# Kernel tuning notes

Measured on AMD Instinct MI355X. Metric: run time of the kernel, lower is better.

## Reference

```python
import jax, jax.numpy as jnp
import numpy as np

# Fixed production-scale dims (see shape_source)
B, R, WIDTH, T, H, W = 8, 12, 2304, 4, 16, 29
REDUCE, HID, NC, ROI_SP, DEPTH = 1024, 512, 60, 7, 2
SR = 2  # roi_align sampling ratio (fixed; torchvision default -1 is roi-adaptive)


def conv2d(x, w, pad):
    return jax.lax.conv_general_dilated(
        x, w, (1, 1), [(pad, pad), (pad, pad)],
        dimension_numbers=('NCHW', 'OIHW', 'NCHW'))


def maxpool_3x3_s2(x):
    return jax.lax.reduce_window(
        x, -jnp.inf, jax.lax.max, (1, 1, 3, 3), (1, 1, 2, 2),
        [(0, 0), (0, 0), (1, 1), (1, 1)])


def bilinear(img, ys, xs):
    # img [C,h,w]; ys, xs [P] -> [C,P]; matches torchvision bilinear_interpolate
    h, w = img.shape[1], img.shape[2]
    valid = (ys >= -1.0) & (ys <= h) & (xs >= -1.0) & (xs <= w)
    y = jnp.clip(ys, 0.0, h - 1.0)
    x = jnp.clip(xs, 0.0, w - 1.0)
    y0f = jnp.floor(y); x0f = jnp.floor(x)
    iy0 = y0f.astype(jnp.int32); ix0 = x0f.astype(jnp.int32)
    iy1 = jnp.minimum(iy0 + 1, h - 1); ix1 = jnp.minimum(ix0 + 1, w - 1)
    ly = y - y0f; lx = x - x0f; hy = 1.0 - ly; hx = 1.0 - lx
    v00 = img[:, iy0, ix0]; v01 = img[:, iy0, ix1]
    v10 = img[:, iy1, ix0]; v11 = img[:, iy1, ix1]
    out = hy * hx * v00 + hy * lx * v01 + ly * hx * v10 + ly * lx * v11
    return jnp.where(valid[None, :], out, 0.0)


def roi_align_one(img, box):
    # img [C,H,W]; box (x1,y1,x2,y2) in feature coords; aligned=False, scale=1
    x1, y1, x2, y2 = box[0], box[1], box[2], box[3]
    rw = jnp.maximum(x2 - x1, 1.0)
    rh = jnp.maximum(y2 - y1, 1.0)
    bw = rw / ROI_SP; bh = rh / ROI_SP
    g = (jnp.arange(ROI_SP, dtype=jnp.float32)[:, None]
         + (jnp.arange(SR, dtype=jnp.float32)[None, :] + 0.5) / SR).reshape(-1)  # [7*SR]
    ys = y1 + g * bh; xs = x1 + g * bw
    n = ROI_SP * SR
    yy = jnp.repeat(ys, n); xx = jnp.tile(xs, n)
    vals = bilinear(img, yy, xx)                       # [C, n*n]
    vals = vals.reshape(img.shape[0], ROI_SP, SR, ROI_SP, SR)
    return vals.mean(axis=(2, 4))                      # [C,7,7]


def hr2o_layer(x, qw, kw, vw, cw, gamma, beta):
    # x [R, HID, Hp, Wp]; non-local attention across ROIs of one image
    q = conv2d(x, qw, 1)
    k = conv2d(x, kw, 1)
    v = conv2d(x, vw, 1)
    att = jnp.einsum('ichw,jchw->ijhw', q, k) / jnp.sqrt(jnp.float32(HID))
    att = jax.nn.softmax(att, axis=1)                  # softmax over key rois
    virt = jnp.einsum('ijhw,jchw->ichw', att, v)
    mu = virt.mean(axis=(1, 2, 3), keepdims=True)      # GroupNorm(1, HID)
    var = virt.var(axis=(1, 2, 3), keepdims=True)
    virt = (virt - mu) / jnp.sqrt(var + 1e-5)
    virt = virt * gamma[None, :, None, None] + beta[None, :, None, None]
    virt = jax.nn.relu(virt)
    virt = conv2d(virt, cw, 1)                         # mlp_1x1=False -> 3x3 pad 1
    return x + virt                                    # dropout inactive in eval


def setup_inputs() -> dict:
    key = jax.random.key(0)
    ks = jax.random.split(key, 14)
    features = jax.random.normal(ks[0], (B, WIDTH, T, H, W), jnp.float32)
    xy = jax.random.uniform(ks[1], (B, R, 2), minval=0.0, maxval=0.6)
    wh = jax.random.uniform(ks[2], (B, R, 2), minval=0.2, maxval=0.4)
    rois = jnp.concatenate([xy, xy + wh], axis=-1)     # normalized x1,y1,x2,y2

    def w_(k, shape, fan_in):
        return jax.random.normal(k, shape, jnp.float32) * (1.0 / np.sqrt(fan_in))

    return {
        'features': features,
        'rois': rois,
        'conv_reduce_w': w_(ks[3], (REDUCE, WIDTH, 1, 1), WIDTH),
        'conv1_w': w_(ks[4], (HID, 2 * REDUCE, 1, 1), 2 * REDUCE),
        'conv2_w': w_(ks[5], (HID, HID, 3, 3), HID * 9),
        'hr2o_qw': w_(ks[6], (DEPTH, HID, HID, 3, 3), HID * 9),
        'hr2o_kw': w_(ks[7], (DEPTH, HID, HID, 3, 3), HID * 9),
        'hr2o_vw': w_(ks[8], (DEPTH, HID, HID, 3, 3), HID * 9),
        'hr2o_cw': w_(ks[9], (DEPTH, HID, HID, 3, 3), HID * 9),
        'hr2o_gamma': jnp.ones((DEPTH, HID), jnp.float32),
        'hr2o_beta': jnp.zeros((DEPTH, HID), jnp.float32),
        'fc1_w': w_(ks[10], (HID, REDUCE), REDUCE),
        'fc2_w': w_(ks[11], (NC, 2 * HID), 2 * HID),
    }


def reference(features, rois, conv_reduce_w, conv1_w, conv2_w,
              hr2o_qw, hr2o_kw, hr2o_vw, hr2o_cw, hr2o_gamma, hr2o_beta,
              fc1_w, fc2_w):
    feats = features.mean(axis=2)                      # AdaptiveAvgPool3d((1,H,W)) over T
    feats = conv2d(feats, conv_reduce_w, 0)            # [B, REDUCE, H, W]

    scale = jnp.array([W, H, W, H], jnp.float32)
    boxes = rois * scale                               # feature-space coords (detached)
    ra = jax.vmap(lambda img, bxs: jax.vmap(lambda b: roi_align_one(img, b))(bxs))(
        feats, boxes)                                  # [B, R, REDUCE, 7, 7]
    roi_feats = ra.max(axis=(-2, -1)).reshape(B * R, REDUCE)  # MaxPool2d(7)

    # broadcast bg + tiled actor, concat on channels (eff_h=H, eff_w=W)
    bg = jnp.broadcast_to(feats[:, None], (B, R, REDUCE, H, W))
    actor = jnp.broadcast_to(
        roi_feats.reshape(B, R, REDUCE)[..., None, None], (B, R, REDUCE, H, W))
    x = jnp.concatenate([bg, actor], axis=2).reshape(B * R, 2 * REDUCE, H, W)
    x = jax.nn.relu(conv2d(x, conv1_w, 0))             # 1x1
    x = jax.nn.relu(conv2d(x, conv2_w, 0))             # 3x3, Conv2d default pad=0
    x = maxpool_3x3_s2(x)                              # [B*R, HID, 7, 14]
    hp, wp = x.shape[2], x.shape[3]
    x = x.reshape(B, R, HID, hp, wp)
    for d in range(DEPTH):
        x = jax.vmap(lambda xi: hr2o_layer(
            xi, hr2o_qw[d], hr2o_kw[d], hr2o_vw[d], hr2o_cw[d],
            hr2o_gamma[d], hr2o_beta[d]))(x)
    high = x.mean(axis=(-2, -1)).reshape(B * R, HID)   # GAP

    out = jax.nn.relu(roi_feats @ fc1_w.T)
    out = jnp.concatenate([out, high], axis=1)
    return out @ fc2_w.T                               # [B*R, NC]
```

## Files before the change

### kernel.cpp

```cpp
#include <hip/hip_runtime.h>
#include <math.h>

#define BB 8
#define RR 12
#define WIDTH 2304
#define TT 4
#define HH 16
#define WW 29
#define HWIN (HH*WW)
#define REDUCE 1024
#define HID 512
#define NC 60
#define DEPTH 2
#define NIMG (BB*RR)
#define OH2 14
#define OW2 27
#define NSP2 (OH2*OW2)
#define PH 7
#define PW 14
#define NSP (PH*PW)
#define ATT_SCALE 0.044194173824159216f

typedef __attribute__((ext_vector_type(8))) short short8;
typedef __attribute__((ext_vector_type(4))) float floatx4;

__device__ __forceinline__ void split2(float v, unsigned short& h, unsigned short& l)
{
    union { float f; unsigned u; } c; c.f = v;
    unsigned hb = c.u & 0xffff0000u;
    h = (unsigned short)(hb >> 16);
    union { float f; unsigned u; } hc; hc.u = hb;
    float r = v - hc.f;
    union { float f; unsigned u; } rc; rc.f = r;
    unsigned ru = rc.u + 0x7fffu + ((rc.u >> 16) & 1u);
    l = (unsigned short)(ru >> 16);
}

__device__ __forceinline__ void gll16(const void* g, void* l)
{
    __builtin_amdgcn_global_load_lds((const __attribute__((address_space(1))) void*)g,
                                     (__attribute__((address_space(3))) void*)l,
                                     16, 0, 0);
}

#define MFMA3(d, ah_, al_, bh_, bl_) \
    d = __builtin_amdgcn_mfma_f32_16x16x32_bf16(ah_, bh_, d, 0, 0, 0); \
    d = __builtin_amdgcn_mfma_f32_16x16x32_bf16(ah_, bl_, d, 0, 0, 0); \
    d = __builtin_amdgcn_mfma_f32_16x16x32_bf16(al_, bh_, d, 0, 0, 0);

template<int TYPE, int NSEL, bool RELU, bool RESID, int WR>
__global__ __launch_bounds__(256, 2)
void tapr_k(const int4* __restrict__ WA0, const int4* __restrict__ WA1, const int4* __restrict__ WA2,
            const ushort* __restrict__ BH, const ushort* __restrict__ BL,
            const float* __restrict__ Res,
            float* __restrict__ Y0, float* __restrict__ Y1, float* __restrict__ Y2)
{
    __shared__ int4 L[2064 + 16 * WR];
    const int tid = threadIdx.x;

    int ch, zp, nb = 0;
    if (TYPE == 0) { ch = blockIdx.x / 48; zp = blockIdx.x % 48; }
    else { ch = blockIdx.x / 192; int r = blockIdx.x % 192; nb = r / 48; zp = r % 48; }
    int sel = 0, m0;
    if (NSEL == 3) { sel = ch >> 2; m0 = (ch & 3) * 128; }
    else m0 = ch * 128;
    const int z0 = zp * 2;

    const int4* WA = (NSEL == 3) ? (sel == 0 ? WA0 : sel == 1 ? WA1 : WA2) : WA0;
    float* Y = (NSEL == 3) ? (sel == 0 ? Y0 : sel == 1 ? Y1 : Y2) : Y0;

    const int lane = tid & 63, wv = tid >> 6;
    const int lrow = lane >> 4, lcol = lane & 15;
    constexpr long ALO = 294912;
    constexpr long PLSTR = (TYPE == 1) ? 472L * 512 : 160L * 512;
    const int pbase = (TYPE == 1) ? (((nb * 112) >> 5) * 29 + ((nb * 112) & 31)) : 0;

    int pbnf[7];
#pragma unroll
    for (int nf = 0; nf < 7; ++nf) {
        int col = nf * 16 + lcol;
        if (TYPE == 0) pbnf[nf] = col;
        else { int gn = nb * 112 + col; pbnf[nf] = (gn >> 5) * 29 + (gn & 31) - pbase; }
    }

    int uR[3], uPl[3], uZi[3]; bool uV[3];
    const ushort* uSrc[3];
#pragma unroll
    for (int it = 0; it < 3; ++it) {
        int u = tid + it * 256;
        uV[it] = (u < 4 * WR);
        int uu = uV[it] ? u : 0;
        uR[it] = uu % WR; uPl[it] = (uu / WR) & 1; uZi[it] = uu / (2 * WR);
        const ushort* P = uPl[it] ? BL : BH;
        uSrc[it] = P + (size_t)(z0 + uZi[it]) * PLSTR + (size_t)(pbase + uR[it]) * 512;
    }

    floatx4 acc[2][2][7];
#pragma unroll
    for (int zi = 0; zi < 2; ++zi)
#pragma unroll
        for (int mf = 0; mf < 2; ++mf)
#pragma unroll
            for (int nf = 0; nf < 7; ++nf) acc[zi][mf][nf] = (floatx4){0.f, 0.f, 0.f, 0.f};

#define BCOPY(CB) { \
    _Pragma("unroll") \
    for (int it = 0; it < 3; ++it) if (uV[it]) { \
        const int4* s = (const int4*)(uSrc[it] + (size_t)(CB) * 32); \
        int4 t0 = s[0], t1 = s[1], t2 = s[2], t3_ = s[3]; \
        int bse = 2064 + uZi[it] * (8 * WR) + uPl[it] * (4 * WR) + uR[it]; \
        L[bse] = t0; L[bse + WR] = t1; L[bse + 2 * WR] = t2; L[bse + 3 * WR] = t3_; \
    } }

#define ASTAGE(KST, BUF) { \
    int k8 = (KST) * 4; \
    _Pragma("unroll") \
    for (int j = 0; j < 4; ++j) { \
        int h = wv * 4 + j, p = h >> 3, g = (h >> 1) & 3, hf = h & 1; \
        gll16(WA + (p ? ALO : 0) + (long)(k8 + g) * 512 + m0 + hf * 64 + lane, \
              L + (BUF) * 1032 + (p * 4 + g) * 129 + hf * 64); \
    } }

#define COMPUTE(BUF, SHV) { \
    const int4* La = L + (BUF) * 1032; \
    short8 ah[2], al[2]; \
    _Pragma("unroll") \
    for (int mf = 0; mf < 2; ++mf) { \
        int au = lrow * 129 + (wv * 2 + mf) * 16 + lcol; \
        ah[mf] = *(const short8*)(La + au); \
        al[mf] = *(const short8*)(La + 516 + au); \
    } \
    _Pragma("unroll") \
    for (int nf = 0; nf < 7; ++nf) { \
        int spl = pbnf[nf] + (SHV); \
        _Pragma("unroll") \
        for (int zi = 0; zi < 2; ++zi) { \
            const int4* Lb = L + 2064 + zi * (8 * WR) + lrow * WR + spl; \
            short8 bh = *(const short8*)(Lb); \
            short8 bl = *(const short8*)(Lb + 4 * WR); \
            _Pragma("unroll") \
            for (int mf = 0; mf < 2; ++mf) { MFMA3(acc[zi][mf][nf], ah[mf], al[mf], bh, bl) } \
        } \
    } }

    BCOPY(0)
    ASTAGE(0, 0)
    __syncthreads();

    int cur = 0;
    for (int cb = 0; cb < 16; ++cb) {
#pragma unroll
        for (int tap = 0; tap < 9; ++tap) {
            const int kst = cb * 9 + tap;
            const int t3 = tap / 3;
            const int shv = (TYPE == 0) ? (t3 * 16 + (tap - t3 * 3)) : (t3 * 29 + (tap - t3 * 3));
            if (kst < 143) ASTAGE(kst + 1, cur ^ 1)
            COMPUTE(cur, shv)
            __syncthreads();
            cur ^= 1;
        }
        if (cb < 15) {
            BCOPY(cb + 1)
            __syncthreads();
        }
    }

#pragma unroll
    for (int zi = 0; zi < 2; ++zi) {
        const int z = z0 + zi;
#pragma unroll
        for (int mf = 0; mf < 2; ++mf) {
            int m = m0 + wv * 32 + mf * 16 + lrow * 4;
#pragma unroll
            for (int nf = 0; nf < 7; ++nf) {
                int col = nf * 16 + lcol;
                int sp, realn; bool ok;
                if (TYPE == 0) { int oh = col >> 4, ow = col & 15; ok = ow < 14; sp = oh * 14 + ow; realn = 98; }
                else { int gn = nb * 112 + col; int oh = gn >> 5, ow = gn & 31; ok = ow < 27; sp = oh * 27 + ow; realn = 378; }
                if (ok) {
#pragma unroll
                    for (int r = 0; r < 4; ++r) {
                        size_t idx = ((size_t)z * 512 + m + r) * realn + sp;
                        float v = acc[zi][mf][nf][r];
                        if (RESID) v += Res[idx];
                        if (RELU) v = fmaxf(v, 0.f);
                        Y[idx] = v;
                    }
                }
            }
        }
    }
#undef BCOPY
#undef ASTAGE
#undef COMPUTE
}

template<int KW, int KSTN, int MTOT, long PLSTR, int NREAL>
__global__ __launch_bounds__(256, 2)
void tapc_k(const int4* __restrict__ WA,
            const ushort* __restrict__ BH, const ushort* __restrict__ BL,
            float* __restrict__ Y)
{
    __shared__ int4 L[3872];
    const int tid = threadIdx.x;
    const int z = blockIdx.z, nb = blockIdx.x;
    const int m0 = blockIdx.y * 128;
    const int lane = tid & 63, wv = tid >> 6;
    const int lrow = lane >> 4, lcol = lane & 15;
    constexpr long ALO = (long)KSTN * 4 * MTOT;

    int nU[2], gU[2]; long pbU[2]; bool vU[2];
#pragma unroll
    for (int it = 0; it < 2; ++it) {
        int u = tid + (it << 8);
        vU[it] = (u < 448);
        int uu = vU[it] ? u : 0;
        nU[it] = uu % 112; gU[it] = uu / 112;
        int gn = nb * 112 + nU[it];
        pbU[it] = min(gn, NREAL - 1);
    }
    const ushort* BHz = BH + (size_t)z * PLSTR;
    const ushort* BLz = BL + (size_t)z * PLSTR;

    floatx4 acc[2][7];
#pragma unroll
    for (int mf = 0; mf < 2; ++mf)
#pragma unroll
        for (int nf = 0; nf < 7; ++nf) acc[mf][nf] = (floatx4){0.f, 0.f, 0.f, 0.f};

    short8 rbh[2], rbl[2];

#define STAGE_ISSUE(KST, BUF) { \
    int k8 = (KST) * 4; \
    _Pragma("unroll") \
    for (int j = 0; j < 4; ++j) { \
        int h = wv * 4 + j, p = h >> 3, g = (h >> 1) & 3, hf = h & 1; \
        gll16(WA + (p ? ALO : 0) + (long)(k8 + g) * MTOT + m0 + hf * 64 + lane, \
              L + (BUF) * 1936 + (p * 4 + g) * 129 + hf * 64); \
    } \
    int ci0 = (KST) << 5; \
    _Pragma("unroll") \
    for (int it = 0; it < 2; ++it) if (vU[it]) { \
        size_t o = (size_t)pbU[it] * KW + ci0 + gU[it] * 8; \
        rbh[it] = *(const short8*)(BHz + o); \
        rbl[it] = *(const short8*)(BLz + o); \
    } }

#define STAGE_WRITE(BUF) { \
    _Pragma("unroll") \
    for (int it = 0; it < 2; ++it) if (vU[it]) { \
        *((short8*)(L + (BUF) * 1936 + 1032 + gU[it] * 113 + nU[it])) = rbh[it]; \
        *((short8*)(L + (BUF) * 1936 + 1484 + gU[it] * 113 + nU[it])) = rbl[it]; \
    } }

#define COMPUTE(BUF) { \
    const int4* Lc = L + (BUF) * 1936; \
    short8 ah[2], al[2]; \
    _Pragma("unroll") \
    for (int mf = 0; mf < 2; ++mf) { \
        int au = lrow * 129 + (wv * 2 + mf) * 16 + lcol; \
        ah[mf] = *(const short8*)(Lc + au); \
        al[mf] = *(const short8*)(Lc + 516 + au); \
    } \
    _Pragma("unroll") \
    for (int nf = 0; nf < 7; ++nf) { \
        int bu = 1032 + lrow * 113 + nf * 16 + lcol; \
        short8 bh = *(const short8*)(Lc + bu); \
        short8 bl = *(const short8*)(Lc + bu + 452); \
        _Pragma("unroll") \
        for (int mf = 0; mf < 2; ++mf) { MFMA3(acc[mf][nf], ah[mf], al[mf], bh, bl) } \
    } }

    STAGE_ISSUE(0, 0)
    STAGE_WRITE(0)
    __syncthreads();

    int cur = 0;
    for (int kst = 0; kst < KSTN; ++kst) {
        int nxt = cur ^ 1;
        bool more = (kst + 1 < KSTN);
        if (more) STAGE_ISSUE(kst + 1, nxt)
        COMPUTE(cur)
        if (more) { STAGE_WRITE(nxt) __syncthreads(); }
        cur = nxt;
    }

#pragma unroll
    for (int mf = 0; mf < 2; ++mf) {
        int m = m0 + wv * 32 + mf * 16 + lrow * 4;
#pragma unroll
        for (int nf = 0; nf < 7; ++nf) {
            int col = nf * 16 + lcol;
            int gn = nb * 112 + col;
            if (gn < NREAL) {
#pragma unroll
                for (int r = 0; r < 4; ++r) {
                    size_t idx = ((size_t)z * MTOT + m + r) * NREAL + gn;
                    Y[idx] = acc[mf][nf][r];
                }
            }
        }
    }
#undef STAGE_ISSUE
#undef STAGE_WRITE
#undef COMPUTE
}

__global__ void prep_w_k(const float* __restrict__ s0, const float* __restrict__ s1,
                         const float* __restrict__ s2, const float* __restrict__ s3,
                         int4* __restrict__ dst)
{
    const int c = blockIdx.y;
    const float* src = (c == 0) ? s0 : (c == 1) ? s1 : (c == 2) ? s2 : s3;
    int4* dh = dst + (size_t)c * 589824;
    int4* dl = dh + 294912;
    int idx = blockIdx.x * 256 + threadIdx.x;
    if (idx >= 294912) return;
    int g8 = idx / 512, m = idx & 511;
    unsigned hw[4], lw[4];
#pragma unroll
    for (int j = 0; j < 4; ++j) {
        int k1 = g8 * 8 + 2 * j, k2 = k1 + 1;
        int cb1 = k1 / 288, r1 = k1 % 288, tp1 = r1 >> 5, ci1 = cb1 * 32 + (r1 & 31);
        int cb2 = k2 / 288, r2 = k2 % 288, tp2 = r2 >> 5, ci2 = cb2 * 32 + (r2 & 31);
        float v1 = src[(size_t)m * 4608 + ci1 * 9 + tp1];
        float v2 = src[(size_t)m * 4608 + ci2 * 9 + tp2];
        unsigned short h0, l0, h1, l1;
        split2(v1, h0, l0); split2(v2, h1, l1);
        hw[j] = (unsigned)h0 | ((unsigned)h1 << 16);
        lw[j] = (unsigned)l0 | ((unsigned)l1 << 16);
    }
    dh[idx] = make_int4(hw[0], hw[1], hw[2], hw[3]);
    dl[idx] = make_int4(lw[0], lw[1], lw[2], lw[3]);
}

__global__ void prep_wg_k(const float* __restrict__ src, int ldw, int M, int K8,
                          int4* __restrict__ dst)
{
    int idx = blockIdx.x * 256 + threadIdx.x;
    if (idx >= K8 * M) return;
    int g8 = idx / M, m = idx % M;
    unsigned hw[4], lw[4];
#pragma unroll
    for (int j = 0; j < 4; ++j) {
        int k1 = g8 * 8 + 2 * j;
        float v1 = src[(size_t)m * ldw + k1];
        float v2 = src[(size_t)m * ldw + k1 + 1];
        unsigned short h0, l0, h1, l1;
        split2(v1, h0, l0); split2(v2, h1, l1);
        hw[j] = (unsigned)h0 | ((unsigned)h1 << 16);
        lw[j] = (unsigned)l0 | ((unsigned)l1 << 16);
    }
    dst[idx] = make_int4(hw[0], hw[1], hw[2], hw[3]);
    dst[(size_t)K8 * M + idx] = make_int4(lw[0], lw[1], lw[2], lw[3]);
}

__global__ __launch_bounds__(256)
void tsplit_k(const float* __restrict__ src, ushort* __restrict__ dh, ushort* __restrict__ dl,
              int C, int S, long zsrc, long zdst)
{
    __shared__ float t[64][65];
    const int c0 = blockIdx.x * 64, s0 = blockIdx.y * 64, z = blockIdx.z;
    const float* sz = src + (size_t)z * zsrc;
    const int tx = threadIdx.x & 63, ty = threadIdx.x >> 6;
#pragma unroll
    for (int i = 0; i < 16; ++i) {
        int cc = i * 4 + ty;
        int c = c0 + cc, s = s0 + tx;
        t[cc][tx] = (c < C && s < S) ? sz[(size_t)c * S + s] : 0.f;
    }
    __syncthreads();
#pragma unroll
    for (int i = 0; i < 16; ++i) {
        int ss = i * 4 + ty;
        int s = s0 + ss, c = c0 + tx;
        if (s < S && c < C) {
            unsigned short h, l;
            split2(t[tx][ss], h, l);
            size_t o = (size_t)z * zdst + (size_t)s * C + c;
            dh[o] = h; dl[o] = l;
        }
    }
}

__global__ __launch_bounds__(256)
void tsplit_c2_k(const float* __restrict__ bg, const float* __restrict__ bias1,
                 ushort* __restrict__ dh, ushort* __restrict__ dl)
{
    __shared__ float t[64][65];
    const int c0 = blockIdx.x * 64, s0 = blockIdx.y * 64, z = blockIdx.z;
    const int b = z / RR;
    const int tx = threadIdx.x & 63, ty = threadIdx.x >> 6;
#pragma unroll
    for (int i = 0; i < 16; ++i) {
        int cc = i * 4 + ty;
        int s = s0 + tx;
        t[cc][tx] = (s < 464) ? bg[((size_t)b * 512 + c0 + cc) * 464 + s] : 0.f;
    }
    __syncthreads();
    const float bv = bias1[z * 512 + c0 + tx];
#pragma unroll
    for (int i = 0; i < 16; ++i) {
        int ss = i * 4 + ty;
        int s = s0 + ss, c = c0 + tx;
        if (s < 472) {
            float v = (s < 464) ? fmaxf(t[tx][ss] + bv, 0.f) : 0.f;
            unsigned short h, l;
            split2(v, h, l);
            size_t o = (size_t)z * 241664 + (size_t)s * 512 + c;
            dh[o] = h; dl[o] = l;
        }
    }
}

__global__ __launch_bounds__(256)
void tsplit_pad_k(const float* __restrict__ x, ushort* __restrict__ dh, ushort* __restrict__ dl)
{
    __shared__ float t[64 * 99];
    const int c0 = blockIdx.x * 64, z = blockIdx.y;
    const int tid = threadIdx.x;
#pragma unroll
    for (int i = 0; i < 25; ++i) {
        int idx = tid + i * 256;
        if (idx < 6272) {
            int c = idx / 98, s = idx % 98;
            t[c * 99 + s] = x[((size_t)z * 512 + c0 + c) * 98 + s];
        }
    }
    __syncthreads();
#pragma unroll
    for (int i = 0; i < 40; ++i) {
        int idx = tid + i * 256;
        int sp = idx >> 6, c = idx & 63;
        int r = sp >> 4, col = sp & 15;
        float v = (r >= 1 && r <= 7 && col >= 1 && col <= 14) ? t[c * 99 + (r - 1) * 14 + col - 1] : 0.f;
        unsigned short h, l;
        split2(v, h, l);
        size_t o = (size_t)z * 81920 + (size_t)sp * 512 + c0 + c;
        dh[o] = h; dl[o] = l;
    }
}

__global__ void tmean_k(const float* __restrict__ f, float* __restrict__ o, int total)
{
    int i = blockIdx.x * blockDim.x + threadIdx.x;
    if (i >= total) return;
    int p = i % HWIN; long bc = i / HWIN;
    const float* src = f + bc * (long)TT * HWIN + p;
    o[i] = (src[0] + src[HWIN] + src[2 * HWIN] + src[3 * HWIN]) * 0.25f;
}

__global__ __launch_bounds__(256)
void roi_align_k(const float* __restrict__ feats, const float* __restrict__ rois,
                 float* __restrict__ roi_feats)
{
    __shared__ int s_o00[196], s_o01[196], s_o10[196], s_o11[196];
    __shared__ float s_w[4][196];
    const int n = blockIdx.x;
    const int b = n / RR;
    const int t = threadIdx.x;
    if (t < 196) {
        float x1 = rois[n * 4 + 0] * WW, y1 = rois[n * 4 + 1] * HH;
        float x2 = rois[n * 4 + 2] * WW, y2 = rois[n * 4 + 3] * HH;
        float rw = fmaxf(x2 - x1, 1.f), rh = fmaxf(y2 - y1, 1.f);
        float bw = rw / 7.f, bh = rh / 7.f;
        int j = t / 14, i = t % 14;
        float gy = (float)(j >> 1) + ((j & 1) + 0.5f) * 0.5f;
        float gx = (float)(i >> 1) + ((i & 1) + 0.5f) * 0.5f;
        float ys = y1 + gy * bh, xs = x1 + gx * bw;
        bool valid = (ys >= -1.f) && (ys <= (float)HH) && (xs >= -1.f) && (xs <= (float)WW);
        float y = fminf(fmaxf(ys, 0.f), (float)(HH - 1));
        float x = fminf(fmaxf(xs, 0.f), (float)(WW - 1));
        float y0f = floorf(y), x0f = floorf(x);
        int iy0 = (int)y0f, ix0 = (int)x0f;
        int iy1 = min(iy0 + 1, HH - 1), ix1 = min(ix0 + 1, WW - 1);
        float ly = y - y0f, lx = x - x0f, hy = 1.f - ly, hx = 1.f - lx;
        float msk = valid ? 1.f : 0.f;
        s_o00[t] = iy0 * WW + ix0; s_o01[t] = iy0 * WW + ix1;
        s_o10[t] = iy1 * WW + ix0; s_o11[t] = iy1 * WW + ix1;
        s_w[0][t] = hy * hx * msk; s_w[1][t] = hy * lx * msk;
        s_w[2][t] = ly * hx * msk; s_w[3][t] = ly * lx * msk;
    }
    __syncthreads();
    for (int c = t; c < REDUCE; c += 256) {
        const float* img = feats + ((long)(b * REDUCE + c)) * HWIN;
        float mx = -INFINITY;
        for (int bin = 0; bin < 49; ++bin) {
            int by_ = bin / 7, bx = bin % 7;
            float s = 0.f;
#pragma unroll
            for (int sy = 0; sy < 2; ++sy)
#pragma unroll
                for (int sx = 0; sx < 2; ++sx) {
                    int ss = (by_ * 2 + sy) * 14 + bx * 2 + sx;
                    s += s_w[0][ss] * img[s_o00[ss]] + s_w[1][ss] * img[s_o01[ss]]
                       + s_w[2][ss] * img[s_o10[ss]] + s_w[3][ss] * img[s_o11[ss]];
                }
            mx = fmaxf(mx, s * 0.25f);
        }
        roi_feats[(long)n * REDUCE + c] = mx;
    }
}

__global__ void dots_k(const float* __restrict__ Xr, const float* __restrict__ Wt,
                       int ldw, int woff, float* __restrict__ Y,
                       int Nrows, int M, int K, int relu)
{
    int idx = blockIdx.x * blockDim.x + threadIdx.x;
    if (idx >= Nrows * M) return;
    int o = idx / Nrows, n = idx % Nrows;
    const float* xr = Xr + (long)n * K;
    const float* w = Wt + (long)o * ldw + woff;
    float acc = 0.f;
    for (int k = 0; k < K; ++k) acc = fmaf(xr[k], w[k], acc);
    if (relu) acc = fmaxf(acc, 0.f);
    Y[(long)n * M + o] = acc;
}

__global__ void maxpool_k(const float* __restrict__ in, float* __restrict__ out, int total)
{
    int idx = blockIdx.x * blockDim.x + threadIdx.x;
    if (idx >= total) return;
    int ow = idx % PW; int r = idx / PW; int oh = r % PH; long nc = r / PH;
    const float* src = in + nc * NSP2;
    float m = -INFINITY;
    for (int kh = 0; kh < 3; ++kh) {
        int ih = oh * 2 - 1 + kh; if (ih < 0 || ih >= OH2) continue;
        for (int kw = 0; kw < 3; ++kw) {
            int iw = ow * 2 - 1 + kw; if (iw < 0 || iw >= OW2) continue;
            m = fmaxf(m, src[ih * OW2 + iw]);
        }
    }
    out[idx] = m;
}

__global__ __launch_bounds__(256)
void att2_k(const float* __restrict__ q, const float* __restrict__ k, float* __restrict__ att)
{
    __shared__ float qs[5376];
    __shared__ float ks[5376];
    __shared__ float sc[1008];
    const int b = blockIdx.x, p0 = blockIdx.y * 7;
    const int tid = threadIdx.x;

    int itI[4], itJ[4], itP[4]; bool itV[4];
#pragma unroll
    for (int r = 0; r < 4; ++r) {
        int item = tid + (r << 8);
        itV[r] = item < 1008;
        int it = itV[r] ? item : 0;
        int ij = it / 7; itP[r] = it % 7;
        itI[r] = ij / 12; itJ[r] = ij % 12;
    }
    float acc[4] = {0.f, 0.f, 0.f, 0.f};

    for (int cc0 = 0; cc0 < 512; cc0 += 64) {
        for (int l = tid; l < 5376; l += 256) {
            int i = l / 448, r = l % 448, c = r / 7, p = r % 7;
            size_t off = ((size_t)(b * 12 + i) * 512 + cc0 + c) * 98 + p0 + p;
            qs[l] = q[off];
            ks[l] = k[off];
        }
        __syncthreads();
#pragma unroll
        for (int r = 0; r < 4; ++r) {
            if (itV[r]) {
                const float* qp = qs + itI[r] * 448 + itP[r];
                const float* kp = ks + itJ[r] * 448 + itP[r];
                float a = acc[r];
#pragma unroll 8
                for (int c = 0; c < 64; ++c) a = fmaf(qp[c * 7], kp[c * 7], a);
                acc[r] = a;
            }
        }
        __syncthreads();
    }
#pragma unroll
    for (int r = 0; r < 4; ++r)
        if (itV[r]) sc[tid + (r << 8)] = acc[r] * ATT_SCALE;
    __syncthreads();
    if (tid < 84) {
        int i = tid / 7, p = tid % 7;
        float m = -INFINITY;
        float v[12];
#pragma unroll
        for (int j = 0; j < 12; ++j) { v[j] = sc[(i * 12 + j) * 7 + p]; m = fmaxf(m, v[j]); }
        float s = 0.f;
#pragma unroll
        for (int j = 0; j < 12; ++j) { v[j] = expf(v[j] - m); s += v[j]; }
        float inv = 1.f / s;
#pragma unroll
        for (int j = 0; j < 12; ++j)
            att[((size_t)(b * 12 + i) * 12 + j) * 98 + p0 + p] = v[j] * inv;
    }
}

__global__ __launch_bounds__(256)
void virt2_k(const float* __restrict__ att, const float* __restrict__ v, float* __restrict__ virt)
{
    __shared__ float as_[14112];
    const int b = blockIdx.x, cb = blockIdx.y;
    const int tid = threadIdx.x;
    for (int l = tid; l < 14112; l += 256) as_[l] = att[(size_t)b * 14112 + l];
    __syncthreads();

    for (int it = tid; it < 6272; it += 256) {
        int c = cb * 64 + it / 98, p = it % 98;
        float o[12];
#pragma unroll
        for (int i = 0; i < 12; ++i) o[i] = 0.f;
#pragma unroll
        for (int j = 0; j < 12; ++j) {
            float vj = v[((size_t)(b * 12 + j) * 512 + c) * 98 + p];
#pragma unroll
            for (int i = 0; i < 12; ++i) o[i] = fmaf(as_[(i * 12 + j) * 98 + p], vj, o[i]);
        }
#pragma unroll
        for (int i = 0; i < 12; ++i)
            virt[((size_t)(b * 12 + i) * 512 + c) * 98 + p] = o[i];
    }
}

__global__ __launch_bounds__(256)
void stats_k(const float* __restrict__ virt, float* __restrict__ mu, float* __restrict__ rstd)
{
    int n = blockIdx.x;
    const float* src = virt + (long)n * HID * NSP;
    float s = 0.f, q = 0.f;
    for (int i = threadIdx.x; i < HID * NSP; i += 256) {
        float v = src[i]; s += v; q = fmaf(v, v, q);
    }
    for (int off = 32; off; off >>= 1) { s += __shfl_down(s, off); q += __shfl_down(q, off); }
    __shared__ float ss[4], sq[4];
    int w = threadIdx.x >> 6;
    if ((threadIdx.x & 63) == 0) { ss[w] = s; sq[w] = q; }
    __syncthreads();
    if (threadIdx.x == 0) {
        float S = ss[0] + ss[1] + ss[2] + ss[3];
        float Q = sq[0] + sq[1] + sq[2] + sq[3];
        const float invN = 1.f / (HID * NSP);
        float m = S * invN;
        float var = Q * invN - m * m;
        mu[n] = m; rstd[n] = rsqrtf(var + 1e-5f);
    }
}

__global__ void norm_k(float* __restrict__ virt, const float* __restrict__ mu,
                       const float* __restrict__ rstd,
                       const float* __restrict__ gamma, const float* __restrict__ beta)
{
    int idx = blockIdx.x * blockDim.x + threadIdx.x;
    const int TOT = NIMG * HID * NSP;
    if (idx >= TOT) return;
    int n = idx / (HID * NSP);
    int c = (idx / NSP) % HID;
    float val = (virt[idx] - mu[n]) * rstd[n] * gamma[c] + beta[c];
    virt[idx] = fmaxf(val, 0.f);
}

__global__ void meanpool_k(const float* __restrict__ x, float* __restrict__ high)
{
    int idx = blockIdx.x * blockDim.x + threadIdx.x;
    if (idx >= NIMG * HID) return;
    const float* src = x + (long)idx * NSP;
    float s = 0.f;
    for (int p = 0; p < NSP; ++p) s += src[p];
    high[idx] = s * (1.f / NSP);
}

__global__ void final_k(const float* __restrict__ fc1o, const float* __restrict__ high,
                        const float* __restrict__ fc2, float* __restrict__ out)
{
    int idx = blockIdx.x * blockDim.x + threadIdx.x;
    if (idx >= NIMG * NC) return;
    int n = idx / NC, o = idx % NC;
    const float* w = fc2 + (long)o * (2 * HID);
    const float* a = fc1o + (long)n * HID;
    const float* h = high + (long)n * HID;
    float acc = 0.f;
    for (int c = 0; c < HID; ++c) acc = fmaf(a[c], w[c], acc);
    for (int c = 0; c < HID; ++c) acc = fmaf(h[c], w[HID + c], acc);
    out[idx] = acc;
}

extern "C" void kernel_launch(void* const* d_in, const int* in_sizes, int n_in,
                              void* d_out, int out_size, void* d_ws, size_t ws_size,
                              hipStream_t stream)
{
    (void)in_sizes; (void)n_in; (void)out_size; (void)ws_size;
    const float* features = (const float*)d_in[0];
    const float* rois     = (const float*)d_in[1];
    const float* w_reduce = (const float*)d_in[2];
    const float* w_conv1  = (const float*)d_in[3];
    const float* w_conv2  = (const float*)d_in[4];
    const float* qw       = (const float*)d_in[5];
    const float* kw       = (const float*)d_in[6];
    const float* vw       = (const float*)d_in[7];
    const float* cw       = (const float*)d_in[8];
    const float* gamma    = (const float*)d_in[9];
    const float* beta     = (const float*)d_in[10];
    const float* fc1      = (const float*)d_in[11];
    const float* fc2      = (const float*)d_in[12];
    float* ws = (float*)d_ws;

    float*  tmean = ws + 0;
    ushort* tmTH  = (ushort*)(ws + 8552448);
    ushort* tmTL  = (ushort*)(ws + 12828672);
    float*  feats = ws + 17104896;
    ushort* ftTH  = (ushort*)(ws + 0);
    ushort* ftTL  = (ushort*)(ws + 1900544);
    ushort* B2H   = (ushort*)(ws + 0);
    ushort* B2L   = (ushort*)(ws + 11599872);
    int4*   WTQ   = (int4*)(ws + 0);
    float*  bg    = ws + 23199744;
    float*  out2  = ws + 23199744;
    float*  qb    = ws + 23199744;
    float*  kb    = ws + 28016640;
    float*  vb    = ws + 32833536;
    ushort* PTH   = (ushort*)(ws + 41779200);
    ushort* PTL   = (ushort*)(ws + 45711360);
    float*  xb    = ws + 49643520;
    float*  virt  = ws + 54460416;
    int4*   WTS   = (int4*)(ws + 59277312);
    float*  rf    = ws + 61636608;
    float*  bias1 = ws + 61734912;
    float*  fc1o  = ws + 61784064;
    float*  attb  = ws + 61833216;
    float*  mu    = ws + 61946112;
    float*  rstd  = ws + 61946240;
    float*  high  = ws + 61946368;

    dim3 blk(256);

    prep_wg_k<<<1152, blk, 0, stream>>>(w_reduce, 2304, 1024, 288, WTS);

    { int tot = BB * WIDTH * HWIN;
      tmean_k<<<(tot + 255) / 256, blk, 0, stream>>>(features, tmean, tot); }

    tsplit_k<<<dim3(36, 8, 8), blk, 0, stream>>>(tmean, tmTH, tmTL, 2304, 464, 1069056, 1069056);

    tapc_k<2304, 72, 1024, 464L * 2304, 464>
        <<<dim3(5, 8, 8), blk, 0, stream>>>(WTS, tmTH, tmTL, feats);

    tsplit_k<<<dim3(16, 8, 8), blk, 0, stream>>>(feats, ftTH, ftTL, 1024, 464, 475136, 475136);

    roi_align_k<<<96, blk, 0, stream>>>(feats, rois, rf);
    dots_k<<<(NIMG * HID + 255) / 256, blk, 0, stream>>>(rf, w_conv1, 2048, 1024, bias1, NIMG, HID, REDUCE, 0);
    dots_k<<<(NIMG * HID + 255) / 256, blk, 0, stream>>>(rf, fc1, 1024, 0, fc1o, NIMG, HID, REDUCE, 1);

    prep_wg_k<<<256, blk, 0, stream>>>(w_conv1, 2048, 512, 128, WTS);
    tapc_k<1024, 32, 512, 464L * 1024, 464>
        <<<dim3(5, 4, 8), blk, 0, stream>>>(WTS, ftTH, ftTL, bg);

    prep_w_k<<<dim3(1152, 1), blk, 0, stream>>>(w_conv2, w_conv2, w_conv2, w_conv2, WTS);
    tsplit_c2_k<<<dim3(8, 8, 96), blk, 0, stream>>>(bg, bias1, B2H, B2L);

    tapr_k<1, 1, true, false, 164><<<768, blk, 0, stream>>>(
        WTS, nullptr, nullptr, B2H, B2L, nullptr, out2, nullptr, nullptr);

    { int tot = NIMG * HID * NSP;
      maxpool_k<<<(tot + 255) / 256, blk, 0, stream>>>(out2, xb, tot); }

    for (int d = 0; d < DEPTH; ++d) {
        long woff = (long)d * HID * HID * 9;
        prep_w_k<<<dim3(1152, 4), blk, 0, stream>>>(qw + woff, kw + woff, vw + woff, cw + woff, WTQ);

        tsplit_pad_k<<<dim3(8, 96), blk, 0, stream>>>(xb, PTH, PTL);
        tapr_k<0, 3, false, false, 160><<<576, blk, 0, stream>>>(
            WTQ, WTQ + 589824, WTQ + 2 * 589824, PTH, PTL, nullptr, qb, kb, vb);

        att2_k<<<dim3(8, 14), blk, 0, stream>>>(qb, kb, attb);
        virt2_k<<<dim3(8, 8), blk, 0, stream>>>(attb, vb, virt);
        stats_k<<<96, blk, 0, stream>>>(virt, mu, rstd);
        { int tot = NIMG * HID * NSP;
          norm_k<<<(tot + 255) / 256, blk, 0, stream>>>(virt, mu, rstd, gamma + d * HID, beta + d * HID); }

        tsplit_pad_k<<<dim3(8, 96), blk, 0, stream>>>(virt, PTH, PTL);
        tapr_k<0, 1, false, true, 160><<<192, blk, 0, stream>>>(
            WTQ + 3 * 589824, nullptr, nullptr, PTH, PTL, xb, xb, nullptr, nullptr);
    }

    meanpool_k<<<(NIMG * HID + 255) / 256, blk, 0, stream>>>(xb, high);
    final_k<<<(NIMG * NC + 255) / 256, blk, 0, stream>>>(fc1o, high, fc2, (float*)d_out);
}
```

Measured before the change: 2.971 ms.

## Retile 3x3 tap conv kernel to full-M 512-thread blocks per image

The tap-based 3x3 conv kernel now has 512-thread blocks, each covering all 512 output channels for a single image (z), instead of 128 channels across two images. Weight staging per block grows fourfold while the activation tile is loaded once per image, and the B-row stride is padded to odd values (161/165) to avoid LDS bank conflicts. This cuts redundant activation loads but halves or quarters the grid size (96–384 blocks). It also needs a much larger dynamic LDS allocation, which may limit occupancy.

```diff
diff --git a/kernel.cpp b/kernel.cpp
--- a/kernel.cpp
+++ b/kernel.cpp
@@ -49,22 +49,18 @@
     d = __builtin_amdgcn_mfma_f32_16x16x32_bf16(al_, bh_, d, 0, 0, 0);
 
 template<int TYPE, int NSEL, bool RELU, bool RESID, int WR>
-__global__ __launch_bounds__(256, 2)
-void tapr_k(const int4* __restrict__ WA0, const int4* __restrict__ WA1, const int4* __restrict__ WA2,
-            const ushort* __restrict__ BH, const ushort* __restrict__ BL,
-            const float* __restrict__ Res,
-            float* __restrict__ Y0, float* __restrict__ Y1, float* __restrict__ Y2)
-{
-    __shared__ int4 L[2064 + 16 * WR];
+__global__ __launch_bounds__(512, 2)
+void tapr2_k(const int4* __restrict__ WA0, const int4* __restrict__ WA1, const int4* __restrict__ WA2,
+             const ushort* __restrict__ BH, const ushort* __restrict__ BL,
+             const float* __restrict__ Res,
+             float* __restrict__ Y0, float* __restrict__ Y1, float* __restrict__ Y2)
+{
+    extern __shared__ int4 L[];
     const int tid = threadIdx.x;
-
-    int ch, zp, nb = 0;
-    if (TYPE == 0) { ch = blockIdx.x / 48; zp = blockIdx.x % 48; }
-    else { ch = blockIdx.x / 192; int r = blockIdx.x % 192; nb = r / 48; zp = r % 48; }
-    int sel = 0, m0;
-    if (NSEL == 3) { sel = ch >> 2; m0 = (ch & 3) * 128; }
-    else m0 = ch * 128;
-    const int z0 = zp * 2;
+    int sel = 0, nb = 0, z;
+    if (TYPE == 1) { nb = blockIdx.x / 96; z = blockIdx.x % 96; }
+    else if (NSEL == 3) { sel = blockIdx.x / 96; z = blockIdx.x % 96; }
+    else { z = blockIdx.x; }
 
     const int4* WA = (NSEL == 3) ? (sel == 0 ? WA0 : sel == 1 ? WA1 : WA2) : WA0;
     float* Y = (NSEL == 3) ? (sel == 0 ? Y0 : sel == 1 ? Y1 : Y2) : Y0;
@@ -73,6 +69,7 @@
     const int lrow = lane >> 4, lcol = lane & 15;
     constexpr long ALO = 294912;
     constexpr long PLSTR = (TYPE == 1) ? 472L * 512 : 160L * 512;
+    constexpr int BOFF = 8208;
     const int pbase = (TYPE == 1) ? (((nb * 112) >> 5) * 29 + ((nb * 112) & 31)) : 0;
 
     int pbnf[7];
@@ -83,64 +80,51 @@
         else { int gn = nb * 112 + col; pbnf[nf] = (gn >> 5) * 29 + (gn & 31) - pbase; }
     }
 
-    int uR[3], uPl[3], uZi[3]; bool uV[3];
-    const ushort* uSrc[3];
-#pragma unroll
-    for (int it = 0; it < 3; ++it) {
-        int u = tid + it * 256;
-        uV[it] = (u < 4 * WR);
-        int uu = uV[it] ? u : 0;
-        uR[it] = uu % WR; uPl[it] = (uu / WR) & 1; uZi[it] = uu / (2 * WR);
-        const ushort* P = uPl[it] ? BL : BH;
-        uSrc[it] = P + (size_t)(z0 + uZi[it]) * PLSTR + (size_t)(pbase + uR[it]) * 512;
-    }
-
-    floatx4 acc[2][2][7];
-#pragma unroll
-    for (int zi = 0; zi < 2; ++zi)
-#pragma unroll
-        for (int mf = 0; mf < 2; ++mf)
-#pragma unroll
-            for (int nf = 0; nf < 7; ++nf) acc[zi][mf][nf] = (floatx4){0.f, 0.f, 0.f, 0.f};
+    const bool uV = (tid < 2 * WR);
+    const int uR = uV ? tid % WR : 0;
+    const int uPl = uV ? tid / WR : 0;
+    const ushort* uSrc = (uPl ? BL : BH) + (size_t)z * PLSTR + (size_t)(pbase + uR) * 512;
+
+    floatx4 acc[4][7];
+#pragma unroll
+    for (int mf = 0; mf < 4; ++mf)
+#pragma unroll
+        for (int nf = 0; nf < 7; ++nf) acc[mf][nf] = (floatx4){0.f, 0.f, 0.f, 0.f};
 
 #define BCOPY(CB) { \
-    _Pragma("unroll") \
-    for (int it = 0; it < 3; ++it) if (uV[it]) { \
-        const int4* s = (const int4*)(uSrc[it] + (size_t)(CB) * 32); \
+    if (uV) { \
+        const int4* s = (const int4*)(uSrc + (size_t)(CB) * 32); \
         int4 t0 = s[0], t1 = s[1], t2 = s[2], t3_ = s[3]; \
-        int bse = 2064 + uZi[it] * (8 * WR) + uPl[it] * (4 * WR) + uR[it]; \
+        int bse = BOFF + uPl * (4 * WR) + uR; \
         L[bse] = t0; L[bse + WR] = t1; L[bse + 2 * WR] = t2; L[bse + 3 * WR] = t3_; \
     } }
 
 #define ASTAGE(KST, BUF) { \
     int k8 = (KST) * 4; \
     _Pragma("unroll") \
-    for (int j = 0; j < 4; ++j) { \
-        int h = wv * 4 + j, p = h >> 3, g = (h >> 1) & 3, hf = h & 1; \
-        gll16(WA + (p ? ALO : 0) + (long)(k8 + g) * 512 + m0 + hf * 64 + lane, \
-              L + (BUF) * 1032 + (p * 4 + g) * 129 + hf * 64); \
+    for (int j = 0; j < 8; ++j) { \
+        int pl = j >> 2, g = j & 3; \
+        gll16(WA + (pl ? ALO : 0) + (long)(k8 + g) * 512 + wv * 64 + lane, \
+              L + (BUF) * 4104 + (pl * 4 + g) * 513 + wv * 64); \
     } }
 
 #define COMPUTE(BUF, SHV) { \
-    const int4* La = L + (BUF) * 1032; \
-    short8 ah[2], al[2]; \
+    const int4* La = L + (BUF) * 4104; \
+    short8 ah[4], al[4]; \
     _Pragma("unroll") \
-    for (int mf = 0; mf < 2; ++mf) { \
-        int au = lrow * 129 + (wv * 2 + mf) * 16 + lcol; \
+    for (int mf = 0; mf < 4; ++mf) { \
+        int au = lrow * 513 + wv * 64 + mf * 16 + lcol; \
         ah[mf] = *(const short8*)(La + au); \
-        al[mf] = *(const short8*)(La + 516 + au); \
+        al[mf] = *(const short8*)(La + 2052 + au); \
     } \
     _Pragma("unroll") \
     for (int nf = 0; nf < 7; ++nf) { \
         int spl = pbnf[nf] + (SHV); \
+        const int4* Lb = L + BOFF + lrow * WR + spl; \
+        short8 bh = *(const short8*)(Lb); \
+        short8 bl = *(const short8*)(Lb + 4 * WR); \
         _Pragma("unroll") \
-        for (int zi = 0; zi < 2; ++zi) { \
-            const int4* Lb = L + 2064 + zi * (8 * WR) + lrow * WR + spl; \
-            short8 bh = *(const short8*)(Lb); \
-            short8 bl = *(const short8*)(Lb + 4 * WR); \
-            _Pragma("unroll") \
-            for (int mf = 0; mf < 2; ++mf) { MFMA3(acc[zi][mf][nf], ah[mf], al[mf], bh, bl) } \
-        } \
+        for (int mf = 0; mf < 4; ++mf) { MFMA3(acc[mf][nf], ah[mf], al[mf], bh, bl) } \
     } }
 
     BCOPY(0)
@@ -166,26 +150,22 @@
     }
 
 #pragma unroll
-    for (int zi = 0; zi < 2; ++zi) {
-        const int z = z0 + zi;
-#pragma unroll
-        for (int mf = 0; mf < 2; ++mf) {
-            int m = m0 + wv * 32 + mf * 16 + lrow * 4;
-#pragma unroll
-            for (int nf = 0; nf < 7; ++nf) {
-                int col = nf * 16 + lcol;
-                int sp, realn; bool ok;
-                if (TYPE == 0) { int oh = col >> 4, ow = col & 15; ok = ow < 14; sp = oh * 14 + ow; realn = 98; }
-                else { int gn = nb * 112 + col; int oh = gn >> 5, ow = gn & 31; ok = ow < 27; sp = oh * 27 + ow; realn = 378; }
-                if (ok) {
-#pragma unroll
-                    for (int r = 0; r < 4; ++r) {
-                        size_t idx = ((size_t)z * 512 + m + r) * realn + sp;
-                        float v = acc[zi][mf][nf][r];
-                        if (RESID) v += Res[idx];
-                        if (RELU) v = fmaxf(v, 0.f);
-                        Y[idx] = v;
-                    }
+    for (int mf = 0; mf < 4; ++mf) {
+        int m = wv * 64 + mf * 16 + lrow * 4;
+#pragma unroll
+        for (int nf = 0; nf < 7; ++nf) {
+            int col = nf * 16 + lcol;
+            int sp, realn; bool ok;
+            if (TYPE == 0) { int oh = col >> 4, ow = col & 15; ok = ow < 14; sp = oh * 14 + ow; realn = 98; }
+            else { int gn = nb * 112 + col; int oh = gn >> 5, ow = gn & 31; ok = ow < 27; sp = oh * 27 + ow; realn = 378; }
+            if (ok) {
+#pragma unroll
+                for (int r = 0; r < 4; ++r) {
+                    size_t idx = ((size_t)z * 512 + m + r) * realn + sp;
+                    float v = acc[mf][nf][r];
+                    if (RESID) v += Res[idx];
+                    if (RELU) v = fmaxf(v, 0.f);
+                    Y[idx] = v;
                 }
             }
         }
@@ -731,6 +711,8 @@
     float*  high  = ws + 61946368;
 
     dim3 blk(256);
+    const size_t LDS0 = (8208 + 8 * 161) * sizeof(int4);
+    const size_t LDS1 = (8208 + 8 * 165) * sizeof(int4);
 
     prep_wg_k<<<1152, blk, 0, stream>>>(w_reduce, 2304, 1024, 288, WTS);
 
@@ -755,7 +737,7 @@
     prep_w_k<<<dim3(1152, 1), blk, 0, stream>>>(w_conv2, w_conv2, w_conv2, w_conv2, WTS);
     tsplit_c2_k<<<dim3(8, 8, 96), blk, 0, stream>>>(bg, bias1, B2H, B2L);
 
-    tapr_k<1, 1, true, false, 164><<<768, blk, 0, stream>>>(
+    tapr2_k<1, 1, true, false, 165><<<384, 512, LDS1, stream>>>(
         WTS, nullptr, nullptr, B2H, B2L, nullptr, out2, nullptr, nullptr);
 
     { int tot = NIMG * HID * NSP;
@@ -766,7 +748,7 @@
         prep_w_k<<<dim3(1152, 4), blk, 0, stream>>>(qw + woff, kw + woff, vw + woff, cw + woff, WTQ);
 
         tsplit_pad_k<<<dim3(8, 96), blk, 0, stream>>>(xb, PTH, PTL);
-        tapr_k<0, 3, false, false, 160><<<576, blk, 0, stream>>>(
+        tapr2_k<0, 3, false, false, 161><<<288, 512, LDS0, stream>>>(
             WTQ, WTQ + 589824, WTQ + 2 * 589824, PTH, PTL, nullptr, qb, kb, vb);
 
         att2_k<<<dim3(8, 14), blk, 0, stream>>>(qb, kb, attb);
@@ -776,7 +758,7 @@
           norm_k<<<(tot + 255) / 256, blk, 0, stream>>>(virt, mu, rstd, gamma + d * HID, beta + d * HID); }
 
         tsplit_pad_k<<<dim3(8, 96), blk, 0, stream>>>(virt, PTH, PTL);
-        tapr_k<0, 1, false, true, 160><<<192, blk, 0, stream>>>(
+        tapr2_k<0, 1, false, true, 161><<<96, 512, LDS0, stream>>>(
             WTQ + 3 * 589824, nullptr, nullptr, PTH, PTL, xb, xb, nullptr, nullptr);
     }
 
```

Result: slower. 3.375 ms (+13.6%).
